# Performance work log

Measured on AMD Instinct MI355X. Metric: run time of the kernel, lower is better.

Reference implementation:

```python
import jax, jax.numpy as jnp
import numpy as np

N_CONN = 21  # n_connections


def setup_inputs() -> dict:
    key = jax.random.key(0)
    landmarks = jax.random.normal(key, (262144, N_CONN, 3), dtype=jnp.float32)
    return {"landmarks": landmarks}


def reference(landmarks) -> jnp.ndarray:
    # Faithful to the TF layer: connections = [(i, j) for i in range(n) for j in range(n)],
    # connection_vectors[k] = landmarks[:, j_k] - landmarks[:, i_k]; the loop only reads
    # indices k < n, which correspond to pairs (0, k), so v_k = p_k - p_0 (v_0 == 0).
    b, n = landmarks.shape[0], N_CONN
    v = landmarks[:, :n, :] - landmarks[:, :1, :]          # (b, n, d)
    dots = jnp.einsum("bid,bjd->bij", v, v)                 # (b, n, n)
    norms = jnp.linalg.norm(v, axis=-1)                     # (b, n)
    cos = dots / (norms[:, :, None] * norms[:, None, :])    # 0/0 -> nan for v_0
    ang = jnp.arccos(cos)                                   # (b, n, n)
    ang = jnp.where(jnp.isnan(ang), jnp.zeros_like(ang), ang)
    # TF concatenates n*n tensors of shape (batch,) along axis -1 (== axis 0),
    # yielding shape (n*n*batch,) ordered angle-major.
    return ang.reshape(b, n * n).T.reshape(-1)
```

## Files before the change

### kernel.cpp

```cpp
#include <hip/hip_runtime.h>

#define NCONN 21
#define TPB 256
#define BPB 256

__global__ __launch_bounds__(TPB, 2) void pv_kernel(const float* __restrict__ in,
                                                    float* __restrict__ out,
                                                    int B) {
    __shared__ float lds[BPB * 64];
    const int tid = threadIdx.x;
    const long long blockBatch = (long long)blockIdx.x * BPB;

    const long long gBase4 = blockBatch * 63 / 4;
    const long long totalF4 = ((long long)B * 63) >> 2;
    const float4* in4 = (const float4*)in;
    #pragma unroll
    for (int it = 0; it < 16; ++it) {
        int t4 = tid + it * TPB;
        if (t4 < (BPB * 63) / 4) {
            long long g4 = gBase4 + t4;
            if (g4 < totalF4) {
                float4 v = in4[g4];
                float vals[4] = {v.x, v.y, v.z, v.w};
                int f = 4 * t4;
                #pragma unroll
                for (int q = 0; q < 4; ++q) {
                    int f2 = f + q;
                    int r  = f2 / 63;
                    int c  = f2 - r * 63;
                    lds[r * 64 + ((c + (r >> 2)) & 63)] = vals[q];
                }
            }
        }
    }
    __syncthreads();

    if (blockBatch + tid < B) {
        float* row = lds + tid * 64;
        const int rot = tid >> 2;
        const float p0x = row[(0 + rot) & 63];
        const float p0y = row[(1 + rot) & 63];
        const float p0z = row[(2 + rot) & 63];
        #pragma unroll
        for (int e = 1; e < NCONN; ++e) {
            const int s0 = (3 * e + 0 + rot) & 63;
            const int s1 = (3 * e + 1 + rot) & 63;
            const int s2 = (3 * e + 2 + rot) & 63;
            float vx = row[s0] - p0x;
            float vy = row[s1] - p0y;
            float vz = row[s2] - p0z;
            float d  = fmaf(vx, vx, fmaf(vy, vy, vz * vz));
            float rr = rsqrtf(d);
            row[s0] = vx * rr;
            row[s1] = vy * rr;
            row[s2] = vz * rr;
        }
    }
    __syncthreads();

    const int l = tid & 63;
    const int w = tid >> 6;
    const int rowb = 4 * l;
    const long long remLL = B - blockBatch;
    const int rem = (int)(remLL < BPB ? remLL : (long long)BPB);
    const bool fullv = (rowb + 4 <= rem);
    float* op = out + blockBatch + rowb;
    const size_t sB = (size_t)B;

    {
        const float4 z4 = make_float4(0.f, 0.f, 0.f, 0.f);
        for (int idx = w; idx < 41; idx += 4) {
            const int p = (idx < 21) ? idx : (idx - 20) * NCONN;
            float* dst = op + (size_t)p * sB;
            if (fullv) {
                *(float4*)dst = z4;
            } else {
                for (int k = 0; rowb + k < rem; ++k) dst[k] = 0.0f;
            }
        }
    }

    for (int i = 1; i < NCONN; ++i) {
        float uix[4], uiy[4], uiz[4];
        #pragma unroll
        for (int k = 0; k < 4; ++k) {
            const float* row = lds + (rowb + k) * 64;
            uix[k] = row[(3 * i + 0 + l) & 63];
            uiy[k] = row[(3 * i + 1 + l) & 63];
            uiz[k] = row[(3 * i + 2 + l) & 63];
        }
        const size_t pibase = (size_t)(i * NCONN) * sB;
        for (int jc = 1; jc <= 17; jc += 4) {
            const int j = jc + w;
            float ang[4];
            #pragma unroll
            for (int k = 0; k < 4; ++k) {
                const float* row = lds + (rowb + k) * 64;
                const float ujx = row[(3 * j + 0 + l) & 63];
                const float ujy = row[(3 * j + 1 + l) & 63];
                const float ujz = row[(3 * j + 2 + l) & 63];
                float c = fmaf(uix[k], ujx, fmaf(uiy[k], ujy, uiz[k] * ujz));
                c = fmaxf(fminf(c, 1.0f), -1.0f);
                float t = fabsf(c);
                float s = sqrtf(1.0f - t);
                float p = fmaf(t, -0.0187293f, 0.0742610f);
                p = fmaf(t, p, -0.2121144f);
                p = fmaf(t, p, 1.5707288f);
                float rr = s * p;
                ang[k] = (c >= 0.0f) ? rr : (3.14159265358979f - rr);
            }
            float* dst = op + pibase + (size_t)j * sB;
            if (fullv) {
                *(float4*)dst = make_float4(ang[0], ang[1], ang[2], ang[3]);
            } else {
                for (int k = 0; rowb + k < rem; ++k) dst[k] = ang[k];
            }
        }
    }
}

extern "C" void kernel_launch(void* const* d_in, const int* in_sizes, int n_in,
                              void* d_out, int out_size, void* d_ws, size_t ws_size,
                              hipStream_t stream) {
    const float* in = (const float*)d_in[0];
    float* out = (float*)d_out;
    const int B = in_sizes[0] / (NCONN * 3);
    const int grid = (B + BPB - 1) / BPB;
    hipLaunchKernelGGL(pv_kernel, dim3(grid), dim3(TPB), 0, stream, in, out, B);
}
```

Baseline: 517.2 us.

## Double block threads, flatten angle loop, swizzle block IDs, use nontemporal stores

Raises threads per block to 512 (8 waves) with the same 256-batch tile, so the global load loop halves and the 400 (i,j) angle outputs are spread over 8 waves through one flattened index loop. It remaps block IDs in groups of 8 (an XCD-style interleave) and writes output with nontemporal float4 stores so the large write stream does not pollute cache. The trade-off is reloading the i-vector from LDS on every output, plus extra register and occupancy pressure from the launch-bounds change.

```diff
diff --git a/kernel.cpp b/kernel.cpp
--- a/kernel.cpp
+++ b/kernel.cpp
@@ -1,21 +1,30 @@
 #include <hip/hip_runtime.h>
 
 #define NCONN 21
-#define TPB 256
+#define TPB 512
 #define BPB 256
 
-__global__ __launch_bounds__(TPB, 2) void pv_kernel(const float* __restrict__ in,
+typedef float f4 __attribute__((ext_vector_type(4)));
+
+__global__ __launch_bounds__(TPB, 4) void pv_kernel(const float* __restrict__ in,
                                                     float* __restrict__ out,
                                                     int B) {
     __shared__ float lds[BPB * 64];
     const int tid = threadIdx.x;
-    const long long blockBatch = (long long)blockIdx.x * BPB;
+
+    const int nwg = gridDim.x;
+    int bid = blockIdx.x;
+    if ((nwg & 7) == 0) {
+        const int cpx = nwg >> 3;
+        bid = (bid & 7) * cpx + (bid >> 3);
+    }
+    const long long blockBatch = (long long)bid * BPB;
 
     const long long gBase4 = blockBatch * 63 / 4;
     const long long totalF4 = ((long long)B * 63) >> 2;
     const float4* in4 = (const float4*)in;
     #pragma unroll
-    for (int it = 0; it < 16; ++it) {
+    for (int it = 0; it < 8; ++it) {
         int t4 = tid + it * TPB;
         if (t4 < (BPB * 63) / 4) {
             long long g4 = gBase4 + t4;
@@ -35,7 +44,7 @@
     }
     __syncthreads();
 
-    if (blockBatch + tid < B) {
+    if (tid < BPB && blockBatch + tid < B) {
         float* row = lds + tid * 64;
         const int rot = tid >> 2;
         const float p0x = row[(0 + rot) & 63];
@@ -68,53 +77,46 @@
     const size_t sB = (size_t)B;
 
     {
-        const float4 z4 = make_float4(0.f, 0.f, 0.f, 0.f);
-        for (int idx = w; idx < 41; idx += 4) {
+        const f4 z4 = {0.f, 0.f, 0.f, 0.f};
+        for (int idx = w; idx < 41; idx += 8) {
             const int p = (idx < 21) ? idx : (idx - 20) * NCONN;
             float* dst = op + (size_t)p * sB;
             if (fullv) {
-                *(float4*)dst = z4;
+                __builtin_nontemporal_store(z4, (f4*)dst);
             } else {
                 for (int k = 0; rowb + k < rem; ++k) dst[k] = 0.0f;
             }
         }
     }
 
-    for (int i = 1; i < NCONN; ++i) {
-        float uix[4], uiy[4], uiz[4];
+    for (int idx = w; idx < 400; idx += 8) {
+        const int i = idx / 20 + 1;
+        const int j = idx - (i - 1) * 20 + 1;
+        f4 ang;
         #pragma unroll
         for (int k = 0; k < 4; ++k) {
             const float* row = lds + (rowb + k) * 64;
-            uix[k] = row[(3 * i + 0 + l) & 63];
-            uiy[k] = row[(3 * i + 1 + l) & 63];
-            uiz[k] = row[(3 * i + 2 + l) & 63];
+            const float uix = row[(3 * i + 0 + l) & 63];
+            const float uiy = row[(3 * i + 1 + l) & 63];
+            const float uiz = row[(3 * i + 2 + l) & 63];
+            const float ujx = row[(3 * j + 0 + l) & 63];
+            const float ujy = row[(3 * j + 1 + l) & 63];
+            const float ujz = row[(3 * j + 2 + l) & 63];
+            float c = fmaf(uix, ujx, fmaf(uiy, ujy, uiz * ujz));
+            c = fmaxf(fminf(c, 1.0f), -1.0f);
+            float t = fabsf(c);
+            float s = sqrtf(1.0f - t);
+            float p = fmaf(t, -0.0187293f, 0.0742610f);
+            p = fmaf(t, p, -0.2121144f);
+            p = fmaf(t, p, 1.5707288f);
+            float rr = s * p;
+            ang[k] = (c >= 0.0f) ? rr : (3.14159265358979f - rr);
         }
-        const size_t pibase = (size_t)(i * NCONN) * sB;
-        for (int jc = 1; jc <= 17; jc += 4) {
-            const int j = jc + w;
-            float ang[4];
-            #pragma unroll
-            for (int k = 0; k < 4; ++k) {
-                const float* row = lds + (rowb + k) * 64;
-                const float ujx = row[(3 * j + 0 + l) & 63];
-                const float ujy = row[(3 * j + 1 + l) & 63];
-                const float ujz = row[(3 * j + 2 + l) & 63];
-                float c = fmaf(uix[k], ujx, fmaf(uiy[k], ujy, uiz[k] * ujz));
-                c = fmaxf(fminf(c, 1.0f), -1.0f);
-                float t = fabsf(c);
-                float s = sqrtf(1.0f - t);
-                float p = fmaf(t, -0.0187293f, 0.0742610f);
-                p = fmaf(t, p, -0.2121144f);
-                p = fmaf(t, p, 1.5707288f);
-                float rr = s * p;
-                ang[k] = (c >= 0.0f) ? rr : (3.14159265358979f - rr);
-            }
-            float* dst = op + pibase + (size_t)j * sB;
-            if (fullv) {
-                *(float4*)dst = make_float4(ang[0], ang[1], ang[2], ang[3]);
-            } else {
-                for (int k = 0; rowb + k < rem; ++k) dst[k] = ang[k];
-            }
+        float* dst = op + (size_t)(i * NCONN + j) * sB;
+        if (fullv) {
+            __builtin_nontemporal_store(ang, (f4*)dst);
+        } else {
+            for (int k = 0; rowb + k < rem; ++k) dst[k] = ang[k];
         }
     }
 }
```

Result: no change. 508.2 us (-1.7%).
